# Kernel tuning notes

Measured on AMD Instinct MI355X. Metric: run time of the kernel, lower is better.

## Reference

```python
import jax, jax.numpy as jnp
import numpy as np

EXPAND = 2
KCONV = 4


def _mamba(x, Win, Wconv, bconv, Wx, Wdt, bdt, Alog, Dskip, Wout):
    # x: (B, C, H, W) -> flatten HW to a sequence, run Mamba (S6) block, reshape back
    B, C, H, W = x.shape
    L = H * W
    Di, Kc = Wconv.shape
    R = Wdt.shape[0]
    N = Alog.shape[1]
    xl = x.reshape(B, C, L).transpose(0, 2, 1)            # (B, L, C)
    xz = xl @ Win                                          # (B, L, 2*Di)
    xs, z = xz[..., :Di], xz[..., Di:]
    xt = xs.transpose(0, 2, 1)                             # (B, Di, L)
    xp = jnp.pad(xt, ((0, 0), (0, 0), (Kc - 1, 0)))        # causal depthwise conv1d
    conv = bconv[None, :, None]
    for k in range(Kc):
        conv = conv + Wconv[:, k][None, :, None] * xp[:, :, k:k + L]
    u = jax.nn.silu(conv).transpose(0, 2, 1)               # (B, L, Di)
    dbc = u @ Wx                                           # (B, L, R+2N)
    dt = jax.nn.softplus(dbc[..., :R] @ Wdt + bdt)         # (B, L, Di)
    Bm = dbc[..., R:R + N]                                 # (B, L, N)
    Cm = dbc[..., R + N:]                                  # (B, L, N)
    A = -jnp.exp(Alog)                                     # (Di, N)
    dA = jnp.exp(dt[..., None] * A)                        # (B, L, Di, N)
    dBx = dt[..., None] * Bm[:, :, None, :] * u[..., None] # (B, L, Di, N)

    def step(h, inp):
        a, bx, c = inp
        h = a * h + bx
        return h, jnp.einsum('bdn,bn->bd', h, c)

    h0 = jnp.zeros((B, Di, N), x.dtype)
    _, ys = jax.lax.scan(step, h0, (jnp.swapaxes(dA, 0, 1), jnp.swapaxes(dBx, 0, 1), jnp.swapaxes(Cm, 0, 1)))
    y = jnp.swapaxes(ys, 0, 1) + u * Dskip                 # (B, L, Di)
    y = y * jax.nn.silu(z)
    return (y @ Wout).transpose(0, 2, 1).reshape(B, C, H, W)


def _resize_bilinear(x, oh, ow):
    # F.interpolate(mode='bilinear', align_corners=True)
    B, C, H, W = x.shape
    ys = jnp.linspace(0.0, H - 1.0, oh)
    xs = jnp.linspace(0.0, W - 1.0, ow)
    y0 = jnp.floor(ys).astype(jnp.int32); y1 = jnp.clip(y0 + 1, 0, H - 1); wy = (ys - y0)[:, None]
    x0 = jnp.floor(xs).astype(jnp.int32); x1 = jnp.clip(x0 + 1, 0, W - 1); wx = (xs - x0)[None, :]
    r0 = x[:, :, y0, :]
    r1 = x[:, :, y1, :]
    top = r0[..., x0] * (1 - wx) + r0[..., x1] * wx
    bot = r1[..., x0] * (1 - wx) + r1[..., x1] * wx
    return top * (1 - wy) + bot * wy


def _mamba_params(key, D, N):
    Di = EXPAND * D
    R = max(1, D // 16)
    ks = jax.random.split(key, 6)
    s = 0.02
    Win = s * jax.random.normal(ks[0], (D, 2 * Di), jnp.float32)
    Wconv = s * jax.random.normal(ks[1], (Di, KCONV), jnp.float32)
    bconv = jnp.zeros((Di,), jnp.float32)
    Wx = s * jax.random.normal(ks[2], (Di, R + 2 * N), jnp.float32)
    Wdt = s * jax.random.normal(ks[3], (R, Di), jnp.float32)
    bdt = s * jax.random.normal(ks[4], (Di,), jnp.float32)
    Alog = jnp.tile(jnp.log(jnp.arange(1, N + 1, dtype=jnp.float32))[None, :], (Di, 1))
    Dskip = jnp.ones((Di,), jnp.float32)
    Wout = s * jax.random.normal(ks[5], (Di, D), jnp.float32)
    return Win, Wconv, bconv, Wx, Wdt, bdt, Alog, Dskip, Wout


def setup_inputs() -> dict:
    key = jax.random.key(0)
    C, B, N = 64, 2, 16
    sizes = [48, 24, 12, 6]
    ks = jax.random.split(key, 16)
    inp = {}
    for i, s in enumerate(sizes):
        inp[f'feat{i}'] = jax.random.normal(ks[i], (B, C, s, s), jnp.float32)
    names = ['Win', 'Wconv', 'bconv', 'Wx', 'Wdt', 'bdt', 'Alog', 'D', 'Wout']
    lvl = [_mamba_params(ks[4 + i], C, N) for i in range(4)]
    for j, nm in enumerate(names):
        inp['lvl_' + nm] = jnp.stack([lvl[i][j] for i in range(4)])
    cr = _mamba_params(ks[8], 4 * C, N)
    for j, nm in enumerate(names):
        inp['cr_' + nm] = cr[j]
    inp['proj_W'] = 0.02 * jax.random.normal(ks[9], (C, 4 * C), jnp.float32)  # 1x1 conv weight (out,in)
    inp['proj_b'] = jnp.zeros((C,), jnp.float32)
    inp['bn_g'] = jnp.ones((C,), jnp.float32)
    inp['bn_b'] = jnp.zeros((C,), jnp.float32)
    inp['bn_m'] = 0.1 * jax.random.normal(ks[10], (C,), jnp.float32)
    inp['bn_v'] = jax.random.uniform(ks[11], (C,), jnp.float32, minval=0.5, maxval=1.5)
    inp['target_h'] = 48
    inp['target_w'] = 48
    return inp


def reference(feat0, feat1, feat2, feat3,
              lvl_Win, lvl_Wconv, lvl_bconv, lvl_Wx, lvl_Wdt, lvl_bdt, lvl_Alog, lvl_D, lvl_Wout,
              cr_Win, cr_Wconv, cr_bconv, cr_Wx, cr_Wdt, cr_bdt, cr_Alog, cr_D, cr_Wout,
              proj_W, proj_b, bn_g, bn_b, bn_m, bn_v, target_h, target_w):
    feats = [feat0, feat1, feat2, feat3]
    processed = []
    for i, f in enumerate(feats):
        f = f + _mamba(f, lvl_Win[i], lvl_Wconv[i], lvl_bconv[i], lvl_Wx[i], lvl_Wdt[i],
                       lvl_bdt[i], lvl_Alog[i], lvl_D[i], lvl_Wout[i])
        processed.append(_resize_bilinear(f, target_h, target_w))
    x = jnp.concatenate(processed, axis=1)                 # (B, 4C, th, tw)
    x = x + _mamba(x, cr_Win, cr_Wconv, cr_bconv, cr_Wx, cr_Wdt, cr_bdt, cr_Alog, cr_D, cr_Wout)
    y = jnp.einsum('bchw,oc->bohw', x, proj_W) + proj_b[None, :, None, None]
    scale = (bn_g / jnp.sqrt(bn_v + 1e-5))[None, :, None, None]
    y = (y - bn_m[None, :, None, None]) * scale + bn_b[None, :, None, None]
    return jax.nn.relu(y)
```

## Files before the change

### kernel.cpp

```cpp
#include <hip/hip_runtime.h>
#include <cmath>

#define DEV __device__ __forceinline__

typedef unsigned short u16;
typedef u16 u16x8 __attribute__((ext_vector_type(8)));
typedef u16 u16x4 __attribute__((ext_vector_type(4)));
typedef short bf16x8 __attribute__((ext_vector_type(8)));
typedef float f32x4 __attribute__((ext_vector_type(4)));

constexpr int B_ = 2;
constexpr int S4[4]    = {48, 24, 12, 6};
constexpr int L4[4]    = {2304, 576, 144, 36};
constexpr int LOFF4[4] = {0, 2304, 2880, 3024};
constexpr int LTOT = 3060;
constexpr int TOFF4[4] = {0, 144, 180, 189};
constexpr int NTT = 192;
constexpr int NCH4[4]   = {72, 18, 5, 2};
constexpr int CHOFF4[4] = {0, 72, 90, 95};
constexpr int NCHL = 97;
constexpr int NCHC = 72;
constexpr int LC = 2304;
constexpr float LOG2E = 1.44269504088896f;

DEV float siluf(float x) { return x / (1.f + __expf(-x)); }
DEV float softplusf(float x) { return fmaxf(x, 0.f) + log1pf(__expf(-fabsf(x))); }
DEV float b2f(u16 x) { union { float f; unsigned u; } v; v.u = ((unsigned)x) << 16; return v.f; }
DEV u16 f2b(float f) {
  union { float f; unsigned u; } v; v.f = f;
  unsigned r = v.u + 0x7fffu + ((v.u >> 16) & 1u);
  return (u16)(r >> 16);
}

__global__ __launch_bounds__(256) void k_prep(
    const float* __restrict__ projW, const float* __restrict__ crWout,
    const float* __restrict__ cWin, const float* __restrict__ cWx,
    u16* __restrict__ WPB, u16* __restrict__ WtB,
    u16* __restrict__ WinT, float* __restrict__ WxT) {
  __shared__ float sm[64 * 65];
  int blk = blockIdx.x;
  int tid = threadIdx.x;
  if (blk < 128) {
    int i = blk * 256 + tid;
    int d = i >> 6, o = i & 63;
    float acc = 0.f;
#pragma unroll 4
    for (int c = 0; c < 256; ++c)
      acc = fmaf(crWout[d * 256 + c], projW[o * 256 + c], acc);
    WPB[o * 512 + d] = f2b(acc);
  } else if (blk < 192) {
    int i = (blk - 128) * 256 + tid;
    WtB[i] = f2b(projW[i]);
  } else if (blk < 256) {
    int t = blk - 192;
    int ct = t & 3, nt = t >> 2;
    int c0 = ct * 64, n0 = nt * 64;
    for (int i = tid; i < 4096; i += 256) {
      int cc = i >> 6, nn = i & 63;
      sm[cc * 65 + nn] = cWin[(size_t)(c0 + cc) * 1024 + n0 + nn];
    }
    __syncthreads();
    for (int i = tid; i < 4096; i += 256) {
      int nn = i >> 6, cc = i & 63;
      WinT[(size_t)(n0 + nn) * 256 + c0 + cc] = f2b(sm[cc * 65 + nn]);
    }
  } else {
    int i = (blk - 256) * 256 + tid;
    int d = i & 511, j = i >> 9;
    WxT[j * 512 + d] = cWx[d * 48 + j];
  }
}

__global__ __launch_bounds__(256) void k_front_lvl(
    const float* __restrict__ f0, const float* __restrict__ f1,
    const float* __restrict__ f2, const float* __restrict__ f3,
    const float* __restrict__ Win,
    const float* __restrict__ Wconv,
    const float* __restrict__ bconv,
    const float* __restrict__ Wx,
    const float* __restrict__ Wdt,
    const float* __restrict__ bdt,
    u16* __restrict__ u_l, u16* __restrict__ dt_l,
    u16* __restrict__ Bm_l, u16* __restrict__ Cm_l, u16* __restrict__ z_l) {
  __shared__ float s_x[64 * 20];
  __shared__ float s_xs[19 * 128];
  __shared__ float s_u[16 * 132];
  __shared__ float s_dbc[16 * 36];
  int bid = blockIdx.x;
  int b = bid / NTT, t = bid - b * NTT;
  int lvl = 0;
  while (lvl < 3 && t >= TOFF4[lvl + 1]) ++lvl;
  int tl = t - TOFF4[lvl];
  int L = L4[lvl], loff = LOFF4[lvl];
  int l0 = tl * 16;
  int nl = min(16, L - l0);
  const float* fx = lvl == 0 ? f0 : lvl == 1 ? f1 : lvl == 2 ? f2 : f3;
  int tid = threadIdx.x;

  for (int i = tid; i < 64 * 20; i += 256) {
    int c = i / 20, r = i - c * 20;
    int l = l0 - 3 + r;
    float v = 0.f;
    if (r < 19 && l >= 0 && l < L) v = fx[(size_t)(b * 64 + c) * L + l];
    s_x[i] = v;
  }
  __syncthreads();
  {
    int j = tid;
    float acc[19];
#pragma unroll
    for (int r = 0; r < 19; ++r) acc[r] = 0.f;
    const float* W = Win + lvl * 64 * 256 + j;
    for (int c = 0; c < 64; ++c) {
      float w = W[c * 256];
#pragma unroll
      for (int r = 0; r < 19; ++r) acc[r] = fmaf(w, s_x[c * 20 + r], acc[r]);
    }
    if (j < 128) {
#pragma unroll
      for (int r = 0; r < 19; ++r) s_xs[r * 128 + j] = acc[r];
    } else {
      int d = j - 128;
      int dti = d >> 4, jj = d & 15;
      for (int r = 3; r < 19; ++r) {
        int l = l0 - 3 + r;
        if (l < l0 + nl)
          z_l[((size_t)(b * 8 + dti) * LTOT + loff + l) * 16 + jj] = f2b(acc[r]);
      }
    }
  }
  __syncthreads();
  for (int i = tid; i < 16 * 128; i += 256) {
    int l = i >> 7, d = i & 127;
    if (l < nl) {
      const float* wc = Wconv + (lvl * 128 + d) * 4;
      float a = bconv[lvl * 128 + d];
#pragma unroll
      for (int k = 0; k < 4; ++k) a = fmaf(wc[k], s_xs[(l + k) * 128 + d], a);
      float uu = siluf(a);
      s_u[l * 132 + d] = uu;
      u_l[((size_t)(b * 8 + (d >> 4)) * LTOT + loff + l0 + l) * 16 + (d & 15)] = f2b(uu);
    }
  }
  __syncthreads();
  for (int i = tid; i < 16 * 36; i += 256) {
    int l = i & 15, jj = i >> 4;
    if (l < nl) {
      const float* wx = Wx + lvl * 128 * 36 + jj;
      float a = 0.f;
      for (int d = 0; d < 128; ++d) a = fmaf(s_u[l * 132 + d], wx[d * 36], a);
      s_dbc[l * 36 + jj] = a;
      if (jj >= 4) {
        int q = jj - 4;
        size_t gb = ((size_t)(b * LTOT) + loff + l0 + l) * 16;
        if (q < 16) Bm_l[gb + q] = f2b(a);
        else        Cm_l[gb + (q - 16)] = f2b(a);
      }
    }
  }
  __syncthreads();
  for (int i = tid; i < 16 * 128; i += 256) {
    int l = i >> 7, d = i & 127;
    if (l < nl) {
      float a = bdt[lvl * 128 + d];
#pragma unroll
      for (int r = 0; r < 4; ++r)
        a = fmaf(s_dbc[l * 36 + r], Wdt[(lvl * 4 + r) * 128 + d], a);
      dt_l[((size_t)(b * 8 + (d >> 4)) * LTOT + loff + l0 + l) * 16 + (d & 15)] =
          f2b(softplusf(a));
    }
  }
}

template <int MODE, int PASSC>
__global__ __launch_bounds__(256) void k_scan(
    const u16* __restrict__ dtb, const u16* __restrict__ ub,
    const u16* __restrict__ Bmb, const u16* __restrict__ Cmb,
    const u16* __restrict__ zb,
    const float* __restrict__ Alog, const float* __restrict__ Dsk,
    float* __restrict__ hloc, float* __restrict__ Ssum,
    const float* __restrict__ hin, u16* __restrict__ yg) {
  constexpr int DI = MODE ? 512 : 128;
  constexpr int NDT = DI / 16;
  constexpr int NB = DI / 64;
  constexpr int NCHT = MODE ? NCHC : NCHL;
  constexpr int LT = MODE ? LC : LTOT;
  __shared__ __align__(16) u16 smem[PASSC ? 7168 : 4608];
  u16* s_dt = smem;
  u16* s_u  = smem + 2048;
  u16* s_B  = smem + 4096;
  u16* s_C  = PASSC ? smem + 4608 : nullptr;
  u16* s_y  = PASSC ? smem + 5120 : nullptr;

  int bid = blockIdx.x;
  int dblk = bid % NB;
  int rem = bid / NB;
  int gc = rem % NCHT;
  int b = rem / NCHT;
  int lvl = 0, ch = gc, Lq = LC, loff = 0;
  if (MODE == 0) {
    while (lvl < 3 && gc >= CHOFF4[lvl + 1]) ++lvl;
    ch = gc - CHOFF4[lvl];
    Lq = L4[lvl];
    loff = LOFF4[lvl];
  }
  int l0 = ch * 32;
  int len = min(32, Lq - l0);
  int labs0 = loff + l0;
  int tid = threadIdx.x;
  int q = tid & 3;
  int dl = (tid >> 2) & 15;
  int ti_l = tid >> 6;
  int dti = dblk * 4 + ti_l;
  int d = dti * 16 + dl;
  int n0 = q * 4;

  for (int ti = 0; ti < 4; ++ti) {
    size_t g2 = ((size_t)(b * NDT + dblk * 4 + ti) * LT + labs0) * 16;
    const u16x8* pdt = (const u16x8*)(dtb + g2);
    const u16x8* pu  = (const u16x8*)(ub + g2);
    for (int i = tid; i < len * 2; i += 256) {
      *(u16x8*)&s_dt[ti * 512 + i * 8] = pdt[i];
      *(u16x8*)&s_u [ti * 512 + i * 8] = pu[i];
    }
  }
  {
    size_t gB = ((size_t)b * LT + labs0) * 16;
    for (int i = tid; i < len * 2; i += 256) {
      *(u16x8*)&s_B[i * 8] = *(const u16x8*)&Bmb[gB + i * 8];
      if (PASSC) *(u16x8*)&s_C[i * 8] = *(const u16x8*)&Cmb[gB + i * 8];
    }
  }
  __syncthreads();

  int ai = (MODE ? d : lvl * 128 + d);
  float4 al = *(const float4*)&Alog[ai * 16 + n0];
  float kA2[4] = {-__expf(al.x) * LOG2E, -__expf(al.y) * LOG2E,
                  -__expf(al.z) * LOG2E, -__expf(al.w) * LOG2E};
  size_t hix = (((size_t)(b * NCHT) + gc) * DI + d) * 16 + n0;
  float h[4] = {0.f, 0.f, 0.f, 0.f};
  if (PASSC) {
    float4 hv = *(const float4*)&hin[hix];
    h[0] = hv.x; h[1] = hv.y; h[2] = hv.z; h[3] = hv.w;
  }
  float dsk = PASSC ? Dsk[ai] : 0.f;
  float ss = 0.f;

  for (int l = 0; l < len; ++l) {
    float dt = b2f(s_dt[ti_l * 512 + l * 16 + dl]);
    float uu = b2f(s_u [ti_l * 512 + l * 16 + dl]);
    float dtu = dt * uu;
    u16x4 Bv = *(const u16x4*)&s_B[l * 16 + n0];
    if (PASSC) {
      u16x4 Cv = *(const u16x4*)&s_C[l * 16 + n0];
      float p = 0.f;
#pragma unroll
      for (int i = 0; i < 4; ++i) {
        float dA = exp2f(kA2[i] * dt);
        h[i] = fmaf(dA, h[i], dtu * b2f(Bv[i]));
        p = fmaf(h[i], b2f(Cv[i]), p);
      }
      p += __shfl_xor(p, 1, 4);
      p += __shfl_xor(p, 2, 4);
      if (q == 0) s_y[l * 64 + ti_l * 16 + dl] = f2b(fmaf(uu, dsk, p));
    } else {
#pragma unroll
      for (int i = 0; i < 4; ++i) {
        float dA = exp2f(kA2[i] * dt);
        h[i] = fmaf(dA, h[i], dtu * b2f(Bv[i]));
      }
      ss += dt;
    }
  }
  if (!PASSC) {
    f32x4 hv = {h[0], h[1], h[2], h[3]};
    *(f32x4*)&hloc[hix] = hv;
    if (q == 0) Ssum[((size_t)(b * NCHT) + gc) * DI + d] = ss;
  } else {
    __syncthreads();
    for (int ti = 0; ti < 4; ++ti) {
      size_t g2 = ((size_t)(b * NDT + dblk * 4 + ti) * LT + labs0) * 16;
      for (int i = tid; i < len * 2; i += 256) {
        u16x8 zv = *(const u16x8*)&zb[g2 + i * 8];
        u16x8 yv = *(const u16x8*)&s_y[(i >> 1) * 64 + ti * 16 + (i & 1) * 8];
        u16x8 o;
#pragma unroll
        for (int j = 0; j < 8; ++j) {
          float z = b2f(zv[j]);
          float gate = z / (1.f + __expf(-z));
          o[j] = f2b(b2f(yv[j]) * gate);
        }
        *(u16x8*)&yg[g2 + i * 8] = o;
      }
    }
  }
}

__global__ __launch_bounds__(256) void k_combine_lvl(
    const float* __restrict__ Alog, const float* __restrict__ hloc,
    const float* __restrict__ Ssum, float* __restrict__ hin) {
  int i = blockIdx.x * 256 + threadIdx.x;
  int n = i & 15, d = (i >> 4) & 127, lvl = (i >> 11) & 3, b = i >> 13;
  float kA2 = -__expf(Alog[(lvl * 128 + d) * 16 + n]) * LOG2E;
  float h = 0.f;
  int nch = NCH4[lvl];
  for (int ch = 0; ch < nch; ++ch) {
    int gc = CHOFF4[lvl] + ch;
    size_t ix = (((size_t)(b * NCHL) + gc) * 128 + d) * 16 + n;
    hin[ix] = h;
    float S = Ssum[((size_t)(b * NCHL) + gc) * 128 + d];
    h = fmaf(exp2f(kA2 * S), h, hloc[ix]);
  }
}

__global__ __launch_bounds__(256) void k_combine_cr(
    const float* __restrict__ Alog, const float* __restrict__ hloc,
    const float* __restrict__ Ssum, float* __restrict__ hin) {
  int i = blockIdx.x * 256 + threadIdx.x;
  int n = i & 15, d = (i >> 4) & 511, b = i >> 13;
  float kA2 = -__expf(Alog[d * 16 + n]) * LOG2E;
  float h = 0.f;
  for (int ch = 0; ch < NCHC; ++ch) {
    size_t ix = (((size_t)(b * NCHC) + ch) * 512 + d) * 16 + n;
    hin[ix] = h;
    float S = Ssum[((size_t)(b * NCHC) + ch) * 512 + d];
    h = fmaf(exp2f(kA2 * S), h, hloc[ix]);
  }
}

__global__ __launch_bounds__(256) void k_out_lvl(
    const u16* __restrict__ yg_l, const float* __restrict__ Wout,
    const float* __restrict__ f0, const float* __restrict__ f1,
    const float* __restrict__ f2, const float* __restrict__ f3,
    float* __restrict__ fout) {
  __shared__ float s_ygT[128 * 20];
  __shared__ float s_o[16 * 64];
  int bid = blockIdx.x;
  int b = bid / NTT, t = bid - b * NTT;
  int lvl = 0;
  while (lvl < 3 && t >= TOFF4[lvl + 1]) ++lvl;
  int tl = t - TOFF4[lvl];
  int L = L4[lvl], loff = LOFF4[lvl];
  int l0 = tl * 16, nl = min(16, L - l0);
  const float* fx = lvl == 0 ? f0 : lvl == 1 ? f1 : lvl == 2 ? f2 : f3;
  int tid = threadIdx.x;
  for (int i = tid; i < 16 * 128; i += 256) {
    int d = i & 127, l = i >> 7;
    float v = 0.f;
    if (l < nl)
      v = b2f(yg_l[((size_t)(b * 8 + (d >> 4)) * LTOT + loff + l0 + l) * 16 + (d & 15)]);
    s_ygT[d * 20 + l] = v;
  }
  __syncthreads();
  {
    int c = tid & 63, lg = (tid >> 6) * 4;
    float acc[4] = {0.f, 0.f, 0.f, 0.f};
    const float* W = Wout + lvl * 128 * 64 + c;
    for (int dq = 0; dq < 128; ++dq) {
      float w = W[dq * 64];
      float4 yv = *(const float4*)&s_ygT[dq * 20 + lg];
      acc[0] = fmaf(w, yv.x, acc[0]);
      acc[1] = fmaf(w, yv.y, acc[1]);
      acc[2] = fmaf(w, yv.z, acc[2]);
      acc[3] = fmaf(w, yv.w, acc[3]);
    }
#pragma unroll
    for (int a = 0; a < 4; ++a) s_o[(lg + a) * 64 + c] = acc[a];
  }
  __syncthreads();
  for (int i = tid; i < 16 * 64; i += 256) {
    int c = i >> 4, l = i & 15;
    if (l < nl)
      fout[((size_t)(b * 64) + c) * LTOT + loff + l0 + l] =
          s_o[l * 64 + c] + fx[((size_t)(b * 64) + c) * L + l0 + l];
  }
}

__global__ __launch_bounds__(256) void k_resize(const float* __restrict__ fout,
                                                u16* __restrict__ xTb) {
  int i = blockIdx.x * 256 + threadIdx.x;
  int ch = i & 255;
  int rem = i >> 8;
  int hw = rem % 2304;
  int b = rem / 2304;
  int oh = hw / 48, ow = hw - oh * 48;
  int lvl = ch >> 6, c = ch & 63;
  int s = S4[lvl];
  const float* base = fout + ((size_t)(b * 64) + c) * LTOT + LOFF4[lvl];
  float scl = (float)(s - 1) * (1.f / 47.f);
  float fy = oh * scl, fxx = ow * scl;
  int y0 = (int)floorf(fy), x0 = (int)floorf(fxx);
  float wy = fy - y0, wx = fxx - x0;
  int y1 = min(y0 + 1, s - 1), x1 = min(x0 + 1, s - 1);
  float v00 = base[y0 * s + x0], v01 = base[y0 * s + x1];
  float v10 = base[y1 * s + x0], v11 = base[y1 * s + x1];
  float top = v00 * (1.f - wx) + v01 * wx;
  float bot = v10 * (1.f - wx) + v11 * wx;
  xTb[i] = f2b(top * (1.f - wy) + bot * wy);
}

__global__ __launch_bounds__(256) void k_gemm_mfma(
    const u16* __restrict__ xT,
    const u16* __restrict__ WT,
    u16* __restrict__ xs_c, u16* __restrict__ z_c) {
  __shared__ __align__(16) u16 s_a[64 * 72];
  __shared__ __align__(16) u16 s_b[128 * 72];
  int bid = blockIdx.x;
  int nj = bid & 7, bm = bid >> 3;
  int tid = threadIdx.x;
  int lane = tid & 63, w = tid >> 6;
  int wm = (w & 1) * 32, wn = (w >> 1) * 64;
  const int m_base = bm * 64;
  const int n_base = nj * 128;

  f32x4 acc[2][4];
#pragma unroll
  for (int mi = 0; mi < 2; ++mi)
#pragma unroll
    for (int ni = 0; ni < 4; ++ni) acc[mi][ni] = {0.f, 0.f, 0.f, 0.f};

  u16x8 ra0, ra1, rb0, rb1, rb2, rb3;
  auto ld = [&](int c0) {
#pragma unroll
    for (int s = 0; s < 2; ++s) {
      int v = s * 256 + tid;
      int row = v >> 3, kc = (v & 7) * 8;
      u16x8 t = *(const u16x8*)&xT[(size_t)(m_base + row) * 256 + c0 + kc];
      if (s == 0) ra0 = t; else ra1 = t;
    }
#pragma unroll
    for (int s = 0; s < 4; ++s) {
      int v = s * 256 + tid;
      int row = v >> 3, kc = (v & 7) * 8;
      u16x8 t = *(const u16x8*)&WT[(size_t)(n_base + row) * 256 + c0 + kc];
      if (s == 0) rb0 = t; else if (s == 1) rb1 = t;
      else if (s == 2) rb2 = t; else rb3 = t;
    }
  };
  auto st = [&]() {
#pragma unroll
    for (int s = 0; s < 2; ++s) {
      int v = s * 256 + tid;
      int row = v >> 3, kc = (v & 7) * 8;
      *(u16x8*)&s_a[row * 72 + kc] = (s == 0) ? ra0 : ra1;
    }
#pragma unroll
    for (int s = 0; s < 4; ++s) {
      int v = s * 256 + tid;
      int row = v >> 3, kc = (v & 7) * 8;
      const u16x8& t = (s == 0) ? rb0 : (s == 1) ? rb1 : (s == 2) ? rb2 : rb3;
      *(u16x8*)&s_b[row * 72 + kc] = t;
    }
  };
  ld(0);
  int mlane = lane & 15, kg = (lane >> 4) * 8;
  for (int kt = 0; kt < 4; ++kt) {
    st();
    __syncthreads();
    if (kt < 3) ld((kt + 1) * 64);
#pragma unroll
    for (int kk = 0; kk < 2; ++kk) {
      int k0 = kk * 32 + kg;
      bf16x8 af[2], bfr[4];
#pragma unroll
      for (int mi = 0; mi < 2; ++mi)
        af[mi] = *(const bf16x8*)&s_a[(wm + mi * 16 + mlane) * 72 + k0];
#pragma unroll
      for (int ni = 0; ni < 4; ++ni)
        bfr[ni] = *(const bf16x8*)&s_b[(wn + ni * 16 + mlane) * 72 + k0];
#pragma unroll
      for (int mi = 0; mi < 2; ++mi)
#pragma unroll
        for (int ni = 0; ni < 4; ++ni)
          acc[mi][ni] = __builtin_amdgcn_mfma_f32_16x16x32_bf16(
              af[mi], bfr[ni], acc[mi][ni], 0, 0, 0);
    }
    __syncthreads();
  }
  int rgrp = (lane >> 4) * 4;
#pragma unroll
  for (int mi = 0; mi < 2; ++mi) {
#pragma unroll
    for (int ni = 0; ni < 4; ++ni) {
      int n = n_base + wn + ni * 16 + mlane;
#pragma unroll
      for (int r = 0; r < 4; ++r) {
        int gm = m_base + wm + mi * 16 + rgrp + r;
        int b = gm >= 2304;
        int l = gm - b * 2304;
        u16 v = f2b(acc[mi][ni][r]);
        if (n < 512) {
          xs_c[((size_t)(b * LC) + l) * 512 + n] = v;
        } else {
          int dz = n - 512;
          z_c[((size_t)(b * 32 + (dz >> 4)) * LC + l) * 16 + (dz & 15)] = v;
        }
      }
    }
  }
}

__global__ __launch_bounds__(1024) void k_mid_cr(
    const u16* __restrict__ xs_c,
    const float* __restrict__ Wconv,
    const float* __restrict__ bconv,
    const float* __restrict__ WxT,
    const float* __restrict__ Wdt,
    const float* __restrict__ bdt, u16* __restrict__ u_c,
    u16* __restrict__ dt_c, u16* __restrict__ Bm_c, u16* __restrict__ Cm_c) {
  __shared__ __align__(16) u16 s_xs[19 * 512];
  __shared__ __align__(16) u16 s_ub[16 * 520];
  __shared__ __align__(16) float s_wx[48 * 132];
  __shared__ float s_dbc[16 * 48];
  int bid = blockIdx.x;
  int b = bid / 144, tl = bid - b * 144;
  int l0 = tl * 16;
  int tid = threadIdx.x;
  for (int i = tid; i < 19 * 64; i += 1024) {
    int r = i >> 6, c8 = (i & 63) * 8;
    int l = l0 - 3 + r;
    u16x8 v = {0, 0, 0, 0, 0, 0, 0, 0};
    if (l >= 0)
      v = *(const u16x8*)&xs_c[((size_t)(b * LC) + l) * 512 + c8];
    *(u16x8*)&s_xs[r * 512 + c8] = v;
  }
  __syncthreads();
  for (int i = tid; i < 16 * 512; i += 1024) {
    int l = i >> 9, d = i & 511;
    const float* wc = Wconv + d * 4;
    float a = bconv[d];
#pragma unroll
    for (int k = 0; k < 4; ++k) a = fmaf(wc[k], b2f(s_xs[(l + k) * 512 + d]), a);
    float uu = siluf(a);
    u16 ub = f2b(uu);
    s_ub[l * 520 + d] = ub;
    u_c[((size_t)(b * 32 + (d >> 4)) * LC + l0 + l) * 16 + (d & 15)] = ub;
  }
  int dl = tid & 15, jj = tid >> 4;
  float a8[8] = {0.f, 0.f, 0.f, 0.f, 0.f, 0.f, 0.f, 0.f};
  for (int kt = 0; kt < 4; ++kt) {
    __syncthreads();
    for (int i = tid; i < 1536; i += 1024) {
      int row = i >> 5, c4 = (i & 31) * 4;
      *(float4*)&s_wx[row * 132 + c4] =
          *(const float4*)&WxT[row * 512 + kt * 128 + c4];
    }
    __syncthreads();
    if (tid < 768) {
      const u16* ur = s_ub + dl * 520 + kt * 128;
      const float* wr = s_wx + jj * 132;
#pragma unroll 4
      for (int kb = 0; kb < 16; ++kb) {
        u16x8 uv = *(const u16x8*)&ur[kb * 8];
        float4 w0 = *(const float4*)&wr[kb * 8];
        float4 w1 = *(const float4*)&wr[kb * 8 + 4];
        a8[0] = fmaf(b2f(uv[0]), w0.x, a8[0]);
        a8[1] = fmaf(b2f(uv[1]), w0.y, a8[1]);
        a8[2] = fmaf(b2f(uv[2]), w0.z, a8[2]);
        a8[3] = fmaf(b2f(uv[3]), w0.w, a8[3]);
        a8[4] = fmaf(b2f(uv[4]), w1.x, a8[4]);
        a8[5] = fmaf(b2f(uv[5]), w1.y, a8[5]);
        a8[6] = fmaf(b2f(uv[6]), w1.z, a8[6]);
        a8[7] = fmaf(b2f(uv[7]), w1.w, a8[7]);
      }
    }
  }
  if (tid < 768) {
    float a = ((a8[0] + a8[1]) + (a8[2] + a8[3])) +
              ((a8[4] + a8[5]) + (a8[6] + a8[7]));
    s_dbc[dl * 48 + jj] = a;
    if (jj >= 16) {
      int q = jj - 16;
      size_t gb = ((size_t)(b * LC) + l0 + dl) * 16;
      if (q < 16) Bm_c[gb + q] = f2b(a);
      else        Cm_c[gb + (q - 16)] = f2b(a);
    }
  }
  __syncthreads();
  for (int i = tid; i < 16 * 512; i += 1024) {
    int l = i >> 9, d = i & 511;
    float a = bdt[d];
#pragma unroll
    for (int r = 0; r < 16; ++r)
      a = fmaf(s_dbc[l * 48 + r], Wdt[r * 512 + d], a);
    dt_c[((size_t)(b * 32 + (d >> 4)) * LC + l0 + l) * 16 + (d & 15)] =
        f2b(softplusf(a));
  }
}

__global__ __launch_bounds__(64) void k_final_mfma(
    const u16* __restrict__ xTb,
    const u16* __restrict__ yg_c,
    const u16* __restrict__ WtB,
    const u16* __restrict__ WPB,
    const float* __restrict__ pb, const float* __restrict__ bng,
    const float* __restrict__ bnb, const float* __restrict__ bnm,
    const float* __restrict__ bnv, float* __restrict__ out) {
  int bm = blockIdx.x;
  int b = bm >= 144;
  int m_base = bm * 16;
  int l_base = m_base - b * 2304;
  int lane = threadIdx.x;
  int mrow = lane & 15;
  int kg = (lane >> 4) * 8;
  f32x4 acc[4];
#pragma unroll
  for (int ni = 0; ni < 4; ++ni) acc[ni] = {0.f, 0.f, 0.f, 0.f};
#pragma unroll
  for (int kt = 0; kt < 8; ++kt) {
    int k0 = kt * 32;
    bf16x8 af = *(const bf16x8*)&xTb[(size_t)(m_base + mrow) * 256 + k0 + kg];
#pragma unroll
    for (int ni = 0; ni < 4; ++ni) {
      bf16x8 bw = *(const bf16x8*)&WtB[(ni * 16 + mrow) * 256 + k0 + kg];
      acc[ni] = __builtin_amdgcn_mfma_f32_16x16x32_bf16(af, bw, acc[ni], 0, 0, 0);
    }
  }
#pragma unroll
  for (int kt = 0; kt < 16; ++kt) {
    int kp = kt * 32 + kg;
    int dt = kp >> 4, j0 = kp & 15;
    bf16x8 af = *(const bf16x8*)
        &yg_c[((size_t)(b * 32 + dt) * LC + l_base + mrow) * 16 + j0];
#pragma unroll
    for (int ni = 0; ni < 4; ++ni) {
      bf16x8 bw = *(const bf16x8*)&WPB[(ni * 16 + mrow) * 512 + kt * 32 + kg];
      acc[ni] = __builtin_amdgcn_mfma_f32_16x16x32_bf16(af, bw, acc[ni], 0, 0, 0);
    }
  }
  int rg = (lane >> 4) * 4;
#pragma unroll
  for (int ni = 0; ni < 4; ++ni) {
    int o = ni * 16 + mrow;
    float bias = pb[o], m = bnm[o], g = bng[o], v = bnv[o], bb2 = bnb[o];
    float scl = g * (1.f / sqrtf(v + 1e-5f));
    float4 r;
    r.x = fmaxf((acc[ni][0] + bias - m) * scl + bb2, 0.f);
    r.y = fmaxf((acc[ni][1] + bias - m) * scl + bb2, 0.f);
    r.z = fmaxf((acc[ni][2] + bias - m) * scl + bb2, 0.f);
    r.w = fmaxf((acc[ni][3] + bias - m) * scl + bb2, 0.f);
    *(float4*)&out[((size_t)(b * 64) + o) * LC + l_base + rg] = r;
  }
}

extern "C" void kernel_launch(void* const* d_in, const int* in_sizes, int n_in,
                              void* d_out, int out_size, void* d_ws,
                              size_t ws_size, hipStream_t stream) {
  (void)in_sizes; (void)n_in; (void)out_size; (void)ws_size;
  const float* f0 = (const float*)d_in[0];
  const float* f1 = (const float*)d_in[1];
  const float* f2 = (const float*)d_in[2];
  const float* f3 = (const float*)d_in[3];
  const float* lWin   = (const float*)d_in[4];
  const float* lWconv = (const float*)d_in[5];
  const float* lbconv = (const float*)d_in[6];
  const float* lWx    = (const float*)d_in[7];
  const float* lWdt   = (const float*)d_in[8];
  const float* lbdt   = (const float*)d_in[9];
  const float* lAlog  = (const float*)d_in[10];
  const float* lD     = (const float*)d_in[11];
  const float* lWout  = (const float*)d_in[12];
  const float* cWin   = (const float*)d_in[13];
  const float* cWconv = (const float*)d_in[14];
  const float* cbconv = (const float*)d_in[15];
  const float* cWx    = (const float*)d_in[16];
  const float* cWdt   = (const float*)d_in[17];
  const float* cbdt   = (const float*)d_in[18];
  const float* cAlog  = (const float*)d_in[19];
  const float* cD     = (const float*)d_in[20];
  const float* cWout  = (const float*)d_in[21];
  const float* projW  = (const float*)d_in[22];
  const float* projb  = (const float*)d_in[23];
  const float* bng    = (const float*)d_in[24];
  const float* bnb    = (const float*)d_in[25];
  const float* bnm    = (const float*)d_in[26];
  const float* bnv    = (const float*)d_in[27];
  float* out = (float*)d_out;

  float* ws = (float*)d_ws;
  size_t off = 0;
  auto allocf = [&](size_t n) { float* p = ws + off; off += (n + 7) & ~(size_t)7; return p; };
  auto allocb = [&](size_t n) { u16* p = (u16*)(ws + off); off += ((n + 1) / 2 + 7) & ~(size_t)7; return p; };

  float* WxT    = allocf(48 * 512);
  float* fout   = allocf((size_t)B_ * 64 * LTOT);
  float* hloc_l = allocf((size_t)B_ * NCHL * 128 * 16);
  float* S_l    = allocf((size_t)B_ * NCHL * 128);
  float* hin_l  = allocf((size_t)B_ * NCHL * 128 * 16);
  float* hloc_c = allocf((size_t)B_ * NCHC * 512 * 16);
  float* S_c    = allocf((size_t)B_ * NCHC * 512);
  float* hin_c  = allocf((size_t)B_ * NCHC * 512 * 16);

  u16* WPB   = allocb(64 * 512);
  u16* WtB   = allocb(64 * 256);
  u16* WinT  = allocb(1024 * 256);
  u16* xTb   = allocb((size_t)B_ * LC * 256);
  u16* u_l2  = allocb((size_t)B_ * 8 * LTOT * 16);
  u16* dt_l2 = allocb((size_t)B_ * 8 * LTOT * 16);
  u16* z_l2  = allocb((size_t)B_ * 8 * LTOT * 16);
  u16* yg_l2 = allocb((size_t)B_ * 8 * LTOT * 16);
  u16* Bm_l2 = allocb((size_t)B_ * LTOT * 16);
  u16* Cm_l2 = allocb((size_t)B_ * LTOT * 16);
  u16* xs_c2 = allocb((size_t)B_ * LC * 512);
  u16* u_c2  = allocb((size_t)B_ * 32 * LC * 16);
  u16* dt_c2 = allocb((size_t)B_ * 32 * LC * 16);
  u16* z_c2  = allocb((size_t)B_ * 32 * LC * 16);
  u16* yg_c2 = allocb((size_t)B_ * 32 * LC * 16);
  u16* Bm_c2 = allocb((size_t)B_ * LC * 16);
  u16* Cm_c2 = allocb((size_t)B_ * LC * 16);

  k_prep<<<352, 256, 0, stream>>>(projW, cWout, cWin, cWx, WPB, WtB, WinT, WxT);

  k_front_lvl<<<B_ * NTT, 256, 0, stream>>>(f0, f1, f2, f3, lWin, lWconv,
                                            lbconv, lWx, lWdt, lbdt, u_l2,
                                            dt_l2, Bm_l2, Cm_l2, z_l2);

  k_scan<0, 0><<<B_ * NCHL * 2, 256, 0, stream>>>(
      dt_l2, u_l2, Bm_l2, Cm_l2, nullptr, lAlog, lD, hloc_l, S_l, nullptr,
      nullptr);
  k_combine_lvl<<<64, 256, 0, stream>>>(lAlog, hloc_l, S_l, hin_l);
  k_scan<0, 1><<<B_ * NCHL * 2, 256, 0, stream>>>(
      dt_l2, u_l2, Bm_l2, Cm_l2, z_l2, lAlog, lD, nullptr, nullptr, hin_l,
      yg_l2);

  k_out_lvl<<<B_ * NTT, 256, 0, stream>>>(yg_l2, lWout, f0, f1, f2, f3, fout);
  k_resize<<<(B_ * 256 * LC) / 256, 256, 0, stream>>>(fout, xTb);

  k_gemm_mfma<<<72 * 8, 256, 0, stream>>>(xTb, WinT, xs_c2, z_c2);
  k_mid_cr<<<B_ * 144, 1024, 0, stream>>>(xs_c2, cWconv, cbconv, WxT, cWdt,
                                          cbdt, u_c2, dt_c2, Bm_c2, Cm_c2);

  k_scan<1, 0><<<B_ * NCHC * 8, 256, 0, stream>>>(
      dt_c2, u_c2, Bm_c2, Cm_c2, nullptr, cAlog, cD, hloc_c, S_c, nullptr,
      nullptr);
  k_combine_cr<<<64, 256, 0, stream>>>(cAlog, hloc_c, S_c, hin_c);
  k_scan<1, 1><<<B_ * NCHC * 8, 256, 0, stream>>>(
      dt_c2, u_c2, Bm_c2, Cm_c2, z_c2, cAlog, cD, nullptr, nullptr, hin_c,
      yg_c2);

  k_final_mfma<<<288, 64, 0, stream>>>(xTb, yg_c2, WtB, WPB, projb, bng, bnb,
                                       bnm, bnv, out);
}
```

Measured before the change: 315.8 us.

## Fuse chunked scan passes and combine into cooperative kernels with grid sync

Replaces the two-pass chunked scan plus separate combine kernel with one cooperative kernel per Mamba stage. Each block computes its chunk's local state, grid-syncs, then rebuilds its own incoming state by serially folding the earlier chunks' summaries before running the output pass with the data still in shared memory. The weight prep work is moved into extra blocks of the level scan, and output projection and resize are merged with a grid barrier. This cuts kernel launches and the re-read of inputs, but adds grid-sync cost, a serial prefix loop that grows with chunk index, and requires every block to be co-resident.

New measurement: 747.7 us. 137% more time.

```diff
diff --git a/kernel.cpp b/kernel.cpp
--- a/kernel.cpp
+++ b/kernel.cpp
@@ -1,5 +1,8 @@
 #include <hip/hip_runtime.h>
+#include <hip/hip_cooperative_groups.h>
 #include <cmath>
+
+namespace cg = cooperative_groups;
 
 #define DEV __device__ __forceinline__
 
@@ -30,45 +33,6 @@
   union { float f; unsigned u; } v; v.f = f;
   unsigned r = v.u + 0x7fffu + ((v.u >> 16) & 1u);
   return (u16)(r >> 16);
-}
-
-__global__ __launch_bounds__(256) void k_prep(
-    const float* __restrict__ projW, const float* __restrict__ crWout,
-    const float* __restrict__ cWin, const float* __restrict__ cWx,
-    u16* __restrict__ WPB, u16* __restrict__ WtB,
-    u16* __restrict__ WinT, float* __restrict__ WxT) {
-  __shared__ float sm[64 * 65];
-  int blk = blockIdx.x;
-  int tid = threadIdx.x;
-  if (blk < 128) {
-    int i = blk * 256 + tid;
-    int d = i >> 6, o = i & 63;
-    float acc = 0.f;
-#pragma unroll 4
-    for (int c = 0; c < 256; ++c)
-      acc = fmaf(crWout[d * 256 + c], projW[o * 256 + c], acc);
-    WPB[o * 512 + d] = f2b(acc);
-  } else if (blk < 192) {
-    int i = (blk - 128) * 256 + tid;
-    WtB[i] = f2b(projW[i]);
-  } else if (blk < 256) {
-    int t = blk - 192;
-    int ct = t & 3, nt = t >> 2;
-    int c0 = ct * 64, n0 = nt * 64;
-    for (int i = tid; i < 4096; i += 256) {
-      int cc = i >> 6, nn = i & 63;
-      sm[cc * 65 + nn] = cWin[(size_t)(c0 + cc) * 1024 + n0 + nn];
-    }
-    __syncthreads();
-    for (int i = tid; i < 4096; i += 256) {
-      int nn = i >> 6, cc = i & 63;
-      WinT[(size_t)(n0 + nn) * 256 + c0 + cc] = f2b(sm[cc * 65 + nn]);
-    }
-  } else {
-    int i = (blk - 256) * 256 + tid;
-    int d = i & 511, j = i >> 9;
-    WxT[j * 512 + d] = cWx[d * 48 + j];
-  }
 }
 
 __global__ __launch_bounds__(256) void k_front_lvl(
@@ -172,27 +136,71 @@
   }
 }
 
-template <int MODE, int PASSC>
-__global__ __launch_bounds__(256) void k_scan(
+template <int MODE>
+__global__ __launch_bounds__(256) void k_scanAC(
     const u16* __restrict__ dtb, const u16* __restrict__ ub,
     const u16* __restrict__ Bmb, const u16* __restrict__ Cmb,
     const u16* __restrict__ zb,
     const float* __restrict__ Alog, const float* __restrict__ Dsk,
     float* __restrict__ hloc, float* __restrict__ Ssum,
-    const float* __restrict__ hin, u16* __restrict__ yg) {
+    u16* __restrict__ yg,
+    const float* __restrict__ projW, const float* __restrict__ crWout,
+    const float* __restrict__ cWin, const float* __restrict__ cWx,
+    u16* __restrict__ WPB, u16* __restrict__ WtB,
+    u16* __restrict__ WinT, float* __restrict__ WxT) {
   constexpr int DI = MODE ? 512 : 128;
   constexpr int NDT = DI / 16;
   constexpr int NB = DI / 64;
   constexpr int NCHT = MODE ? NCHC : NCHL;
   constexpr int LT = MODE ? LC : LTOT;
-  __shared__ __align__(16) u16 smem[PASSC ? 7168 : 4608];
+  constexpr int NSCAN = B_ * NCHT * NB;
+  __shared__ __align__(16) u16 smem[7168];
+  __shared__ float sm_t[(MODE == 0) ? 64 * 65 : 8];
   u16* s_dt = smem;
   u16* s_u  = smem + 2048;
   u16* s_B  = smem + 4096;
-  u16* s_C  = PASSC ? smem + 4608 : nullptr;
-  u16* s_y  = PASSC ? smem + 5120 : nullptr;
+  u16* s_C  = smem + 4608;
+  u16* s_y  = smem + 5120;
+  cg::grid_group gridg = cg::this_grid();
 
   int bid = blockIdx.x;
+  int tid = threadIdx.x;
+
+  if (MODE == 0 && bid >= NSCAN) {
+    int blk = bid - NSCAN;
+    if (blk < 128) {
+      int i = blk * 256 + tid;
+      int d = i >> 6, o = i & 63;
+      float acc = 0.f;
+#pragma unroll 4
+      for (int c = 0; c < 256; ++c)
+        acc = fmaf(crWout[d * 256 + c], projW[o * 256 + c], acc);
+      WPB[o * 512 + d] = f2b(acc);
+    } else if (blk < 192) {
+      int i = (blk - 128) * 256 + tid;
+      WtB[i] = f2b(projW[i]);
+    } else if (blk < 256) {
+      int t = blk - 192;
+      int ct = t & 3, nt = t >> 2;
+      int c0 = ct * 64, n0 = nt * 64;
+      for (int i = tid; i < 4096; i += 256) {
+        int cc = i >> 6, nn = i & 63;
+        sm_t[cc * 65 + nn] = cWin[(size_t)(c0 + cc) * 1024 + n0 + nn];
+      }
+      __syncthreads();
+      for (int i = tid; i < 4096; i += 256) {
+        int nn = i >> 6, cc = i & 63;
+        WinT[(size_t)(n0 + nn) * 256 + c0 + cc] = f2b(sm_t[cc * 65 + nn]);
+      }
+    } else {
+      int i = (blk - 256) * 256 + tid;
+      int d = i & 511, j = i >> 9;
+      WxT[j * 512 + d] = cWx[d * 48 + j];
+    }
+    gridg.sync();
+    return;
+  }
+
   int dblk = bid % NB;
   int rem = bid / NB;
   int gc = rem % NCHT;
@@ -207,7 +215,6 @@
   int l0 = ch * 32;
   int len = min(32, Lq - l0);
   int labs0 = loff + l0;
-  int tid = threadIdx.x;
   int q = tid & 3;
   int dl = (tid >> 2) & 15;
   int ti_l = tid >> 6;
@@ -228,7 +235,7 @@
     size_t gB = ((size_t)b * LT + labs0) * 16;
     for (int i = tid; i < len * 2; i += 256) {
       *(u16x8*)&s_B[i * 8] = *(const u16x8*)&Bmb[gB + i * 8];
-      if (PASSC) *(u16x8*)&s_C[i * 8] = *(const u16x8*)&Cmb[gB + i * 8];
+      *(u16x8*)&s_C[i * 8] = *(const u16x8*)&Cmb[gB + i * 8];
     }
   }
   __syncthreads();
@@ -239,11 +246,6 @@
                   -__expf(al.z) * LOG2E, -__expf(al.w) * LOG2E};
   size_t hix = (((size_t)(b * NCHT) + gc) * DI + d) * 16 + n0;
   float h[4] = {0.f, 0.f, 0.f, 0.f};
-  if (PASSC) {
-    float4 hv = *(const float4*)&hin[hix];
-    h[0] = hv.x; h[1] = hv.y; h[2] = hv.z; h[3] = hv.w;
-  }
-  float dsk = PASSC ? Dsk[ai] : 0.f;
   float ss = 0.f;
 
   for (int l = 0; l < len; ++l) {
@@ -251,152 +253,140 @@
     float uu = b2f(s_u [ti_l * 512 + l * 16 + dl]);
     float dtu = dt * uu;
     u16x4 Bv = *(const u16x4*)&s_B[l * 16 + n0];
-    if (PASSC) {
-      u16x4 Cv = *(const u16x4*)&s_C[l * 16 + n0];
-      float p = 0.f;
-#pragma unroll
-      for (int i = 0; i < 4; ++i) {
-        float dA = exp2f(kA2[i] * dt);
-        h[i] = fmaf(dA, h[i], dtu * b2f(Bv[i]));
-        p = fmaf(h[i], b2f(Cv[i]), p);
-      }
-      p += __shfl_xor(p, 1, 4);
-      p += __shfl_xor(p, 2, 4);
-      if (q == 0) s_y[l * 64 + ti_l * 16 + dl] = f2b(fmaf(uu, dsk, p));
-    } else {
-#pragma unroll
-      for (int i = 0; i < 4; ++i) {
-        float dA = exp2f(kA2[i] * dt);
-        h[i] = fmaf(dA, h[i], dtu * b2f(Bv[i]));
-      }
-      ss += dt;
-    }
-  }
-  if (!PASSC) {
+#pragma unroll
+    for (int i = 0; i < 4; ++i) {
+      float dA = exp2f(kA2[i] * dt);
+      h[i] = fmaf(dA, h[i], dtu * b2f(Bv[i]));
+    }
+    ss += dt;
+  }
+  {
     f32x4 hv = {h[0], h[1], h[2], h[3]};
     *(f32x4*)&hloc[hix] = hv;
     if (q == 0) Ssum[((size_t)(b * NCHT) + gc) * DI + d] = ss;
-  } else {
-    __syncthreads();
-    for (int ti = 0; ti < 4; ++ti) {
-      size_t g2 = ((size_t)(b * NDT + dblk * 4 + ti) * LT + labs0) * 16;
-      for (int i = tid; i < len * 2; i += 256) {
-        u16x8 zv = *(const u16x8*)&zb[g2 + i * 8];
-        u16x8 yv = *(const u16x8*)&s_y[(i >> 1) * 64 + ti * 16 + (i & 1) * 8];
-        u16x8 o;
-#pragma unroll
-        for (int j = 0; j < 8; ++j) {
-          float z = b2f(zv[j]);
-          float gate = z / (1.f + __expf(-z));
-          o[j] = f2b(b2f(yv[j]) * gate);
-        }
-        *(u16x8*)&yg[g2 + i * 8] = o;
+  }
+  __threadfence();
+  gridg.sync();
+
+  int chbase = (MODE == 0) ? CHOFF4[lvl] : 0;
+  float hp[4] = {0.f, 0.f, 0.f, 0.f};
+  for (int c2 = chbase; c2 < gc; ++c2) {
+    size_t bb = ((size_t)(b * NCHT) + c2) * DI + d;
+    float S = Ssum[bb];
+    float4 hl = *(const float4*)&hloc[bb * 16 + n0];
+#pragma unroll
+    for (int i = 0; i < 4; ++i)
+      hp[i] = fmaf(exp2f(kA2[i] * S), hp[i], ((const float*)&hl)[i]);
+  }
+
+  float dsk = Dsk[ai];
+  for (int l = 0; l < len; ++l) {
+    float dt = b2f(s_dt[ti_l * 512 + l * 16 + dl]);
+    float uu = b2f(s_u [ti_l * 512 + l * 16 + dl]);
+    float dtu = dt * uu;
+    u16x4 Bv = *(const u16x4*)&s_B[l * 16 + n0];
+    u16x4 Cv = *(const u16x4*)&s_C[l * 16 + n0];
+    float p = 0.f;
+#pragma unroll
+    for (int i = 0; i < 4; ++i) {
+      float dA = exp2f(kA2[i] * dt);
+      hp[i] = fmaf(dA, hp[i], dtu * b2f(Bv[i]));
+      p = fmaf(hp[i], b2f(Cv[i]), p);
+    }
+    p += __shfl_xor(p, 1, 4);
+    p += __shfl_xor(p, 2, 4);
+    if (q == 0) s_y[l * 64 + ti_l * 16 + dl] = f2b(fmaf(uu, dsk, p));
+  }
+  __syncthreads();
+  for (int ti = 0; ti < 4; ++ti) {
+    size_t g2 = ((size_t)(b * NDT + dblk * 4 + ti) * LT + labs0) * 16;
+    for (int i = tid; i < len * 2; i += 256) {
+      u16x8 zv = *(const u16x8*)&zb[g2 + i * 8];
+      u16x8 yv = *(const u16x8*)&s_y[(i >> 1) * 64 + ti * 16 + (i & 1) * 8];
+      u16x8 o;
+#pragma unroll
+      for (int j = 0; j < 8; ++j) {
+        float z = b2f(zv[j]);
+        float gate = z / (1.f + __expf(-z));
+        o[j] = f2b(b2f(yv[j]) * gate);
       }
+      *(u16x8*)&yg[g2 + i * 8] = o;
     }
   }
 }
 
-__global__ __launch_bounds__(256) void k_combine_lvl(
-    const float* __restrict__ Alog, const float* __restrict__ hloc,
-    const float* __restrict__ Ssum, float* __restrict__ hin) {
-  int i = blockIdx.x * 256 + threadIdx.x;
-  int n = i & 15, d = (i >> 4) & 127, lvl = (i >> 11) & 3, b = i >> 13;
-  float kA2 = -__expf(Alog[(lvl * 128 + d) * 16 + n]) * LOG2E;
-  float h = 0.f;
-  int nch = NCH4[lvl];
-  for (int ch = 0; ch < nch; ++ch) {
-    int gc = CHOFF4[lvl] + ch;
-    size_t ix = (((size_t)(b * NCHL) + gc) * 128 + d) * 16 + n;
-    hin[ix] = h;
-    float S = Ssum[((size_t)(b * NCHL) + gc) * 128 + d];
-    h = fmaf(exp2f(kA2 * S), h, hloc[ix]);
-  }
-}
-
-__global__ __launch_bounds__(256) void k_combine_cr(
-    const float* __restrict__ Alog, const float* __restrict__ hloc,
-    const float* __restrict__ Ssum, float* __restrict__ hin) {
-  int i = blockIdx.x * 256 + threadIdx.x;
-  int n = i & 15, d = (i >> 4) & 511, b = i >> 13;
-  float kA2 = -__expf(Alog[d * 16 + n]) * LOG2E;
-  float h = 0.f;
-  for (int ch = 0; ch < NCHC; ++ch) {
-    size_t ix = (((size_t)(b * NCHC) + ch) * 512 + d) * 16 + n;
-    hin[ix] = h;
-    float S = Ssum[((size_t)(b * NCHC) + ch) * 512 + d];
-    h = fmaf(exp2f(kA2 * S), h, hloc[ix]);
-  }
-}
-
-__global__ __launch_bounds__(256) void k_out_lvl(
+__global__ __launch_bounds__(256) void k_out_resize(
     const u16* __restrict__ yg_l, const float* __restrict__ Wout,
     const float* __restrict__ f0, const float* __restrict__ f1,
     const float* __restrict__ f2, const float* __restrict__ f3,
-    float* __restrict__ fout) {
+    float* __restrict__ fout, u16* __restrict__ xTb) {
   __shared__ float s_ygT[128 * 20];
   __shared__ float s_o[16 * 64];
+  cg::grid_group gridg = cg::this_grid();
   int bid = blockIdx.x;
-  int b = bid / NTT, t = bid - b * NTT;
-  int lvl = 0;
-  while (lvl < 3 && t >= TOFF4[lvl + 1]) ++lvl;
-  int tl = t - TOFF4[lvl];
-  int L = L4[lvl], loff = LOFF4[lvl];
-  int l0 = tl * 16, nl = min(16, L - l0);
-  const float* fx = lvl == 0 ? f0 : lvl == 1 ? f1 : lvl == 2 ? f2 : f3;
   int tid = threadIdx.x;
-  for (int i = tid; i < 16 * 128; i += 256) {
-    int d = i & 127, l = i >> 7;
-    float v = 0.f;
-    if (l < nl)
-      v = b2f(yg_l[((size_t)(b * 8 + (d >> 4)) * LTOT + loff + l0 + l) * 16 + (d & 15)]);
-    s_ygT[d * 20 + l] = v;
-  }
-  __syncthreads();
-  {
-    int c = tid & 63, lg = (tid >> 6) * 4;
-    float acc[4] = {0.f, 0.f, 0.f, 0.f};
-    const float* W = Wout + lvl * 128 * 64 + c;
-    for (int dq = 0; dq < 128; ++dq) {
-      float w = W[dq * 64];
-      float4 yv = *(const float4*)&s_ygT[dq * 20 + lg];
-      acc[0] = fmaf(w, yv.x, acc[0]);
-      acc[1] = fmaf(w, yv.y, acc[1]);
-      acc[2] = fmaf(w, yv.z, acc[2]);
-      acc[3] = fmaf(w, yv.w, acc[3]);
-    }
-#pragma unroll
-    for (int a = 0; a < 4; ++a) s_o[(lg + a) * 64 + c] = acc[a];
-  }
-  __syncthreads();
-  for (int i = tid; i < 16 * 64; i += 256) {
-    int c = i >> 4, l = i & 15;
-    if (l < nl)
-      fout[((size_t)(b * 64) + c) * LTOT + loff + l0 + l] =
-          s_o[l * 64 + c] + fx[((size_t)(b * 64) + c) * L + l0 + l];
-  }
-}
-
-__global__ __launch_bounds__(256) void k_resize(const float* __restrict__ fout,
-                                                u16* __restrict__ xTb) {
-  int i = blockIdx.x * 256 + threadIdx.x;
-  int ch = i & 255;
-  int rem = i >> 8;
-  int hw = rem % 2304;
-  int b = rem / 2304;
-  int oh = hw / 48, ow = hw - oh * 48;
-  int lvl = ch >> 6, c = ch & 63;
-  int s = S4[lvl];
-  const float* base = fout + ((size_t)(b * 64) + c) * LTOT + LOFF4[lvl];
-  float scl = (float)(s - 1) * (1.f / 47.f);
-  float fy = oh * scl, fxx = ow * scl;
-  int y0 = (int)floorf(fy), x0 = (int)floorf(fxx);
-  float wy = fy - y0, wx = fxx - x0;
-  int y1 = min(y0 + 1, s - 1), x1 = min(x0 + 1, s - 1);
-  float v00 = base[y0 * s + x0], v01 = base[y0 * s + x1];
-  float v10 = base[y1 * s + x0], v11 = base[y1 * s + x1];
-  float top = v00 * (1.f - wx) + v01 * wx;
-  float bot = v10 * (1.f - wx) + v11 * wx;
-  xTb[i] = f2b(top * (1.f - wy) + bot * wy);
+  if (bid < B_ * NTT) {
+    int b = bid / NTT, t = bid - b * NTT;
+    int lvl = 0;
+    while (lvl < 3 && t >= TOFF4[lvl + 1]) ++lvl;
+    int tl = t - TOFF4[lvl];
+    int L = L4[lvl], loff = LOFF4[lvl];
+    int l0 = tl * 16, nl = min(16, L - l0);
+    const float* fx = lvl == 0 ? f0 : lvl == 1 ? f1 : lvl == 2 ? f2 : f3;
+    for (int i = tid; i < 16 * 128; i += 256) {
+      int d = i & 127, l = i >> 7;
+      float v = 0.f;
+      if (l < nl)
+        v = b2f(yg_l[((size_t)(b * 8 + (d >> 4)) * LTOT + loff + l0 + l) * 16 + (d & 15)]);
+      s_ygT[d * 20 + l] = v;
+    }
+    __syncthreads();
+    {
+      int c = tid & 63, lg = (tid >> 6) * 4;
+      float acc[4] = {0.f, 0.f, 0.f, 0.f};
+      const float* W = Wout + lvl * 128 * 64 + c;
+      for (int dq = 0; dq < 128; ++dq) {
+        float w = W[dq * 64];
+        float4 yv = *(const float4*)&s_ygT[dq * 20 + lg];
+        acc[0] = fmaf(w, yv.x, acc[0]);
+        acc[1] = fmaf(w, yv.y, acc[1]);
+        acc[2] = fmaf(w, yv.z, acc[2]);
+        acc[3] = fmaf(w, yv.w, acc[3]);
+      }
+#pragma unroll
+      for (int a = 0; a < 4; ++a) s_o[(lg + a) * 64 + c] = acc[a];
+    }
+    __syncthreads();
+    for (int i = tid; i < 16 * 64; i += 256) {
+      int c = i >> 4, l = i & 15;
+      if (l < nl)
+        fout[((size_t)(b * 64) + c) * LTOT + loff + l0 + l] =
+            s_o[l * 64 + c] + fx[((size_t)(b * 64) + c) * L + l0 + l];
+    }
+  }
+  __threadfence();
+  gridg.sync();
+  int total = B_ * 2304 * 256;
+  for (int i = bid * 256 + tid; i < total; i += gridDim.x * 256) {
+    int ch = i & 255;
+    int rem = i >> 8;
+    int hw = rem % 2304;
+    int b = rem / 2304;
+    int oh = hw / 48, ow = hw - oh * 48;
+    int lvl = ch >> 6, c = ch & 63;
+    int s = S4[lvl];
+    const float* base = fout + ((size_t)(b * 64) + c) * LTOT + LOFF4[lvl];
+    float scl = (float)(s - 1) * (1.f / 47.f);
+    float fy = oh * scl, fxx = ow * scl;
+    int y0 = (int)floorf(fy), x0 = (int)floorf(fxx);
+    float wy = fy - y0, wx = fxx - x0;
+    int y1 = min(y0 + 1, s - 1), x1 = min(x0 + 1, s - 1);
+    float v00 = base[y0 * s + x0], v01 = base[y0 * s + x1];
+    float v10 = base[y1 * s + x0], v11 = base[y1 * s + x1];
+    float top = v00 * (1.f - wx) + v01 * wx;
+    float bot = v10 * (1.f - wx) + v11 * wx;
+    xTb[i] = f2b(top * (1.f - wy) + bot * wy);
+  }
 }
 
 __global__ __launch_bounds__(256) void k_gemm_mfma(
@@ -686,10 +676,8 @@
   float* fout   = allocf((size_t)B_ * 64 * LTOT);
   float* hloc_l = allocf((size_t)B_ * NCHL * 128 * 16);
   float* S_l    = allocf((size_t)B_ * NCHL * 128);
-  float* hin_l  = allocf((size_t)B_ * NCHL * 128 * 16);
   float* hloc_c = allocf((size_t)B_ * NCHC * 512 * 16);
   float* S_c    = allocf((size_t)B_ * NCHC * 512);
-  float* hin_c  = allocf((size_t)B_ * NCHC * 512 * 16);
 
   u16* WPB   = allocb(64 * 512);
   u16* WtB   = allocb(64 * 256);
@@ -709,34 +697,51 @@
   u16* Bm_c2 = allocb((size_t)B_ * LC * 16);
   u16* Cm_c2 = allocb((size_t)B_ * LC * 16);
 
-  k_prep<<<352, 256, 0, stream>>>(projW, cWout, cWin, cWx, WPB, WtB, WinT, WxT);
-
   k_front_lvl<<<B_ * NTT, 256, 0, stream>>>(f0, f1, f2, f3, lWin, lWconv,
                                             lbconv, lWx, lWdt, lbdt, u_l2,
                                             dt_l2, Bm_l2, Cm_l2, z_l2);
 
-  k_scan<0, 0><<<B_ * NCHL * 2, 256, 0, stream>>>(
-      dt_l2, u_l2, Bm_l2, Cm_l2, nullptr, lAlog, lD, hloc_l, S_l, nullptr,
-      nullptr);
-  k_combine_lvl<<<64, 256, 0, stream>>>(lAlog, hloc_l, S_l, hin_l);
-  k_scan<0, 1><<<B_ * NCHL * 2, 256, 0, stream>>>(
-      dt_l2, u_l2, Bm_l2, Cm_l2, z_l2, lAlog, lD, nullptr, nullptr, hin_l,
-      yg_l2);
-
-  k_out_lvl<<<B_ * NTT, 256, 0, stream>>>(yg_l2, lWout, f0, f1, f2, f3, fout);
-  k_resize<<<(B_ * 256 * LC) / 256, 256, 0, stream>>>(fout, xTb);
+  {
+    const u16 *a0 = dt_l2, *a1 = u_l2, *a2 = Bm_l2, *a3 = Cm_l2, *a4 = z_l2;
+    const float *a5 = lAlog, *a6 = lD;
+    float *a7 = hloc_l, *a8 = S_l;
+    u16* a9 = yg_l2;
+    const float *p0 = projW, *p1 = cWout, *p2 = cWin, *p3 = cWx;
+    u16 *p4 = WPB, *p5 = WtB, *p6 = WinT;
+    float* p7 = WxT;
+    void* args[] = {&a0, &a1, &a2, &a3, &a4, &a5, &a6, &a7, &a8, &a9,
+                    &p0, &p1, &p2, &p3, &p4, &p5, &p6, &p7};
+    hipLaunchCooperativeKernel((void*)k_scanAC<0>, dim3(B_ * NCHL * 2 + 352),
+                               dim3(256), args, 0, stream);
+  }
+
+  {
+    const u16* a0 = yg_l2;
+    const float *a1 = lWout, *a2 = f0, *a3 = f1, *a4 = f2, *a5 = f3;
+    float* a6 = fout;
+    u16* a7 = xTb;
+    void* args[] = {&a0, &a1, &a2, &a3, &a4, &a5, &a6, &a7};
+    hipLaunchCooperativeKernel((void*)k_out_resize, dim3(512), dim3(256), args,
+                               0, stream);
+  }
 
   k_gemm_mfma<<<72 * 8, 256, 0, stream>>>(xTb, WinT, xs_c2, z_c2);
   k_mid_cr<<<B_ * 144, 1024, 0, stream>>>(xs_c2, cWconv, cbconv, WxT, cWdt,
                                           cbdt, u_c2, dt_c2, Bm_c2, Cm_c2);
 
-  k_scan<1, 0><<<B_ * NCHC * 8, 256, 0, stream>>>(
-      dt_c2, u_c2, Bm_c2, Cm_c2, nullptr, cAlog, cD, hloc_c, S_c, nullptr,
-      nullptr);
-  k_combine_cr<<<64, 256, 0, stream>>>(cAlog, hloc_c, S_c, hin_c);
-  k_scan<1, 1><<<B_ * NCHC * 8, 256, 0, stream>>>(
-      dt_c2, u_c2, Bm_c2, Cm_c2, z_c2, cAlog, cD, nullptr, nullptr, hin_c,
-      yg_c2);
+  {
+    const u16 *a0 = dt_c2, *a1 = u_c2, *a2 = Bm_c2, *a3 = Cm_c2, *a4 = z_c2;
+    const float *a5 = cAlog, *a6 = cD;
+    float *a7 = hloc_c, *a8 = S_c;
+    u16* a9 = yg_c2;
+    const float *p0 = nullptr, *p1 = nullptr, *p2 = nullptr, *p3 = nullptr;
+    u16 *p4 = nullptr, *p5 = nullptr, *p6 = nullptr;
+    float* p7 = nullptr;
+    void* args[] = {&a0, &a1, &a2, &a3, &a4, &a5, &a6, &a7, &a8, &a9,
+                    &p0, &p1, &p2, &p3, &p4, &p5, &p6, &p7};
+    hipLaunchCooperativeKernel((void*)k_scanAC<1>, dim3(B_ * NCHC * 8),
+                               dim3(256), args, 0, stream);
+  }
 
   k_final_mfma<<<288, 64, 0, stream>>>(xTb, yg_c2, WtB, WPB, projb, bng, bnb,
                                        bnm, bnv, out);
```
